# Kernel optimization log

Hardware: AMD Instinct MI355X
Metric: run time of the kernel (lower is better)

Reference implementation:

```python
import jax, jax.numpy as jnp
import numpy as np

# Skeleton structure (start, end) connections
REAL_CONNECTIONS = [(0,1),(1,2),(2,3),(3,4),(1,5),(5,6),(6,7),(7,8),(8,9),(8,13),(8,17),(8,21),(8,25),(9,10),(10,11),(11,12),(13,14),(14,15),(15,16),(17,18),(18,19),(19,20),(21,22),(22,23),(23,24),(25,26),(26,27),(27,28),(4,29),(29,30),(29,34),(29,38),(29,42),(29,46),(30,31),(31,32),(32,33),(34,35),(35,36),(36,37),(38,39),(39,40),(40,41),(42,43),(43,44),(44,45),(46,47),(47,48),(48,49)]

def _bone_ranges():
    # dict insertion order matters only for iteration; result is a sum so order-free
    ranges = {(0,1):(0.05,0.15),(1,2):(0.1,0.2),(1,5):(0.1,0.2),(2,3):(0.2,0.35),(3,4):(0.2,0.35),(5,6):(0.2,0.35),(6,7):(0.2,0.35),(4,8):(0.05,0.15),(7,29):(0.05,0.15)}
    for s, e in REAL_CONNECTIONS:
        if 8 <= s < 50 and 8 <= e < 50:
            ranges[(s, e)] = (0.01, 0.08)
    return ranges

_BR = _bone_ranges()
BONE_S = np.array([k[0] for k in _BR], np.int32)
BONE_E = np.array([k[1] for k in _BR], np.int32)
BONE_MIN = np.array([v[0] for v in _BR.values()], np.float32)
BONE_MAX = np.array([v[1] for v in _BR.values()], np.float32)

SYM_L = np.array([8 + i for i in range(21)] + [2, 3, 4], np.int32)
SYM_R = np.array([29 + i for i in range(21)] + [5, 6, 7], np.int32)

ANG_A = np.array([1, 1, 2, 5], np.int32)
ANG_B = np.array([2, 5, 3, 6], np.int32)
ANG_C = np.array([3, 6, 4, 7], np.int32)

CONN_S = np.array([c[0] for c in REAL_CONNECTIONS], np.int32)
CONN_E = np.array([c[1] for c in REAL_CONNECTIONS], np.int32)

DEG = np.float32(180.0 / np.pi)
EPS = np.float32(1e-12)

def _relu(x):
    return jnp.maximum(x, 0.0)

def _normalize(v):
    n = jnp.linalg.norm(v, axis=-1, keepdims=True)
    return v / jnp.maximum(n, EPS)

def setup_inputs() -> dict:
    key = jax.random.key(0)
    k1, k2 = jax.random.split(key)
    B, S, D = 64, 2048, 150
    pred_poses = jax.random.normal(k1, (B, S, D), dtype=jnp.float32)
    target_poses = jax.random.normal(k2, (B, S, D), dtype=jnp.float32)
    return {"pred_poses": pred_poses, "target_poses": target_poses}

def reference(pred_poses, target_poses):
    B, S, _ = pred_poses.shape
    J = pred_poses.reshape(B, S, 50, 3)
    T = target_poses.reshape(B, S, 50, 3)

    # ---- bone length loss (49 constrained bones, one gathered pass) ----
    bv = J[:, :, BONE_E] - J[:, :, BONE_S]                 # [B,S,49,3]
    bl = jnp.linalg.norm(bv, axis=-1)                      # [B,S,49]
    bone_pen = _relu(bl - BONE_MAX) + _relu(BONE_MIN - bl)
    bone_loss = bone_pen.mean()  # == sum over bones of per-bone mean / n_bones

    # ---- joint angle loss (4 triples) ----
    v1 = _normalize(J[:, :, ANG_A] - J[:, :, ANG_B])       # [B,S,4,3]
    v2 = _normalize(J[:, :, ANG_C] - J[:, :, ANG_B])
    cos = jnp.clip(jnp.sum(v1 * v2, axis=-1), -1.0, 1.0)
    deg = jnp.arccos(cos) * DEG
    angle_loss = (_relu(30.0 - deg) + _relu(deg - 150.0)).mean()

    # ---- symmetry loss (24 pairs) ----
    L = J[:, :, SYM_L]                                     # [B,S,24,3]
    R = J[:, :, SYM_R]
    x_sym = jnp.abs(L[..., 0] + R[..., 0])                 # [B,S,24]
    yz_sim = jnp.abs(L[..., 1:] - R[..., 1:]).mean(axis=-1)
    symmetry_loss = (x_sym + yz_sim).mean()

    # ---- temporal consistency ----
    vel = J[:, 1:] - J[:, :-1]                             # [B,S-1,50,3]
    acc = vel[:, 1:] - vel[:, :-1]
    temporal_loss = jnp.linalg.norm(acc, axis=-1).mean() + 0.5 * jnp.linalg.norm(vel, axis=-1).mean()

    # ---- supervised bone-length consistency (all 49 connections) ----
    tb = jnp.linalg.norm(T[:, :, CONN_E] - T[:, :, CONN_S], axis=-1)
    pb = jnp.linalg.norm(J[:, :, CONN_E] - J[:, :, CONN_S], axis=-1)
    supervised_loss = jnp.abs(pb - tb).mean()

    total = (1.0 * bone_loss + 0.5 * angle_loss + 0.3 * symmetry_loss
             + 0.2 * temporal_loss + supervised_loss)
    return bone_loss, angle_loss, symmetry_loss, temporal_loss, supervised_loss, total
```

## Files before the change

### kernel.cpp

```cpp
#include <hip/hip_runtime.h>
#include <math.h>

#define TPB 512
#define CH  32
#define CPB 8

static constexpr int B_     = 64;
static constexpr int S_     = 2048;
static constexpr int TOTAL  = B_ * S_;
static constexpr int NCHUNK = TOTAL / CH;
static constexpr int NBLK   = NCHUNK / CPB;
static constexpr int SAMPB  = 600;
static constexpr int PREDB  = (CH + 2) * SAMPB;
static constexpr int TGTB   = CH * SAMPB;
static constexpr int CHB    = PREDB + TGTB;
static constexpr int NSLICE = 39;
static constexpr int BUFB   = NSLICE * 1024;
static constexpr long TOTB  = (long)TOTAL * SAMPB;

__constant__ int US_[51] = {0,1,1,2,3,5,6,4,7,7,4,
    8,8,8,8,8,9,10,11,13,14,
    15,17,18,19,21,22,23,25,26,27,
    29,29,29,29,29,30,31,32,34,35,
    36,38,39,40,42,43,44,46,47,48};
__constant__ int UE_[51] = {1,2,5,3,4,6,7,8,29,8,29,
    9,13,17,21,25,10,11,12,14,15,
    16,18,19,20,22,23,24,26,27,28,
    30,34,38,42,46,31,32,33,35,36,
    37,39,40,41,43,44,45,47,48,49};
__constant__ float UMIN11_[11] = {0.05f,0.1f,0.1f,0.2f,0.2f,0.2f,0.2f,0.05f,0.05f,-1e9f,-1e9f};
__constant__ float UMAX11_[11] = {0.15f,0.2f,0.2f,0.35f,0.35f,0.35f,0.35f,0.15f,0.15f,1e9f,1e9f};
__constant__ float WSUP11_[11] = {1.f,1.f,1.f,1.f,1.f,1.f,1.f,0.f,0.f,1.f,1.f};
__constant__ int SL_[24] = {8,9,10,11,12,13,14,15,16,17,18,19,20,21,22,23,24,25,26,27,28,2,3,4};
__constant__ int SR_[24] = {29,30,31,32,33,34,35,36,37,38,39,40,41,42,43,44,45,46,47,48,49,5,6,7};
__constant__ int AJ_[4] = {1,1,2,5};
__constant__ int BJ_[4] = {2,5,3,6};
__constant__ int CJ_[4] = {3,6,4,7};

struct F3 { float x, y, z; };
__device__ __forceinline__ F3 ld3(const float* p) { return *(const F3*)p; }
#define SQRTF __builtin_amdgcn_sqrtf

typedef const __attribute__((address_space(1))) void* gas_t;
typedef __attribute__((address_space(3))) void* las_t;

__global__ __launch_bounds__(TPB, 4) void pose_main(
    const float* __restrict__ pred, const float* __restrict__ tgt,
    float* __restrict__ part)
{
    __shared__ __align__(16) char LDS[2 * BUFB];

    const int tid = threadIdx.x;
    const int blk = blockIdx.x;
    const int li  = tid & 15;
    const int g   = tid >> 4;

    const int   uOs0 = US_[g] * 3, uOe0 = UE_[g] * 3;
    const float uMn0 = (g < 11) ? UMIN11_[g] : 0.01f;
    const float uMx0 = (g < 11) ? UMAX11_[g] : 0.08f;
    const float uW0  = (g < 11) ? WSUP11_[g] : 1.f;
    const bool  u1_on = (g < 19);
    const int   k1   = u1_on ? g + 32 : 50;
    const int   uOs1 = US_[k1] * 3, uOe1 = UE_[k1] * 3;
    const bool sy_on = (g < 24);
    const int  ksy = sy_on ? g : 0;
    const int  syL = SL_[ksy] * 3, syR = SR_[ksy] * 3;
    const int aAo = AJ_[g & 3] * 3, aBo = BJ_[g & 3] * 3, aCo = CJ_[g & 3] * 3;
    const int  tO0 = g * 3;
    const int  tO1 = (g + 32) * 3;
    const bool t1_on = (g < 18);

    float a_bone = 0.f, a_ang = 0.f, a_sym = 0.f, a_vel = 0.f, a_acc = 0.f, a_sup = 0.f;

    const int w      = tid >> 6;
    const int lane16 = (tid & 63) << 4;
    auto stage = [&](int cidx, char* lbuf) {
        const long nb = (long)cidx * TGTB;
        const char* pb = (const char*)pred + nb;
        const char* tb = (const char*)tgt  + nb - PREDB;
        const long prem = TOTB - nb - 16;
        #pragma unroll
        for (int s = 0; s < 5; ++s) {
            const int slice = w + s * 8;
            if (slice < NSLICE) {
                const long o = (long)slice * 1024 + lane16;
                const char* src = (o < PREDB)
                    ? pb + (o > prem ? prem : o)
                    : tb + (o > (long)(CHB - 16) ? (long)(CHB - 16) : o);
                __builtin_amdgcn_global_load_lds((gas_t)src, (las_t)(lbuf + slice * 1024), 16, 0, 0);
            }
        }
    };

    const int c0 = blk * CPB;
    stage(c0, LDS);

    #pragma unroll
    for (int c = 0; c < CPB; ++c) {
        char* curb = LDS + (c & 1) * BUFB;
        char* nxtb = LDS + ((c & 1) ^ 1) * BUFB;
        if (c + 1 < CPB) {
            stage(c0 + c + 1, nxtb);
            if (w < 7) asm volatile("s_waitcnt vmcnt(5)" ::: "memory");
            else       asm volatile("s_waitcnt vmcnt(4)" ::: "memory");
        } else {
            asm volatile("s_waitcnt vmcnt(0)" ::: "memory");
        }
        __builtin_amdgcn_s_barrier();
        __builtin_amdgcn_sched_barrier(0);

        const float* Jl = (const float*)curb;
        const float* Tl = Jl + PREDB / 4;
        const int s_base = ((c0 + c) * CH) & (S_ - 1);

        #pragma unroll
        for (int h = 0; h < 2; ++h) {
            const int sb = (li + h * 16) * 150;
            const float* Jp = Jl + sb;
            const float* Tp = Tl + sb;

            auto edge = [&](int so, int eo, float mn, float mx, float wsup) {
                const F3 je = ld3(Jp + eo), js = ld3(Jp + so);
                const float dx = je.x - js.x, dy = je.y - js.y, dz = je.z - js.z;
                const float pb = SQRTF(dx * dx + dy * dy + dz * dz);
                a_bone += fmaxf(pb - mx, 0.f) + fmaxf(mn - pb, 0.f);
                const F3 te = ld3(Tp + eo), ts = ld3(Tp + so);
                const float tx = te.x - ts.x, ty = te.y - ts.y, tz = te.z - ts.z;
                const float tb = SQRTF(tx * tx + ty * ty + tz * tz);
                a_sup += wsup * fabsf(pb - tb);
            };
            edge(uOs0, uOe0, uMn0, uMx0, uW0);
            if (u1_on) edge(uOs1, uOe1, 0.01f, 0.08f, 1.f);

            if (sy_on) {
                const F3 L = ld3(Jp + syL), R = ld3(Jp + syR);
                a_sym += fabsf(L.x + R.x) + 0.5f * (fabsf(L.y - R.y) + fabsf(L.z - R.z));
            }

            if (g < 4) {
                const F3 A = ld3(Jp + aAo), Bb = ld3(Jp + aBo), C = ld3(Jp + aCo);
                const float v1x = A.x - Bb.x, v1y = A.y - Bb.y, v1z = A.z - Bb.z;
                const float v2x = C.x - Bb.x, v2y = C.y - Bb.y, v2z = C.z - Bb.z;
                const float n12 = (v1x*v1x + v1y*v1y + v1z*v1z) * (v2x*v2x + v2y*v2y + v2z*v2z);
                const float inv = __frsqrt_rn(fmaxf(n12, 1e-24f));
                float cosv = (v1x*v2x + v1y*v2y + v1z*v2z) * inv;
                cosv = fminf(fmaxf(cosv, -1.f), 1.f);
                const float deg = acosf(cosv) * 57.29577951308232f;
                a_ang += fmaxf(30.f - deg, 0.f) + fmaxf(deg - 150.f, 0.f);
            }

            {
                const int sidx = s_base + li + h * 16;
                const bool v_ok = sidx < S_ - 1;
                const bool a_ok = sidx < S_ - 2;
                auto temporal = [&](int off) {
                    const F3 p0 = ld3(Jp + off), p1 = ld3(Jp + off + 150), p2 = ld3(Jp + off + 300);
                    if (v_ok) {
                        const float vx = p1.x - p0.x, vy = p1.y - p0.y, vz = p1.z - p0.z;
                        a_vel += SQRTF(vx*vx + vy*vy + vz*vz);
                        if (a_ok) {
                            const float ax = p2.x - 2.f*p1.x + p0.x;
                            const float ay = p2.y - 2.f*p1.y + p0.y;
                            const float az = p2.z - 2.f*p1.z + p0.z;
                            a_acc += SQRTF(ax*ax + ay*ay + az*az);
                        }
                    }
                };
                temporal(tO0);
                if (t1_on) temporal(tO1);
            }
        }

        asm volatile("" ::: "memory");
        __builtin_amdgcn_s_barrier();
    }

    float vals[6] = {a_bone, a_ang, a_sym, a_vel, a_acc, a_sup};
    #pragma unroll
    for (int k = 0; k < 6; ++k)
        #pragma unroll
        for (int off = 32; off > 0; off >>= 1)
            vals[k] += __shfl_down(vals[k], off, 64);

    float* red = (float*)LDS;
    const int lane = tid & 63;
    if (lane == 0) {
        #pragma unroll
        for (int k = 0; k < 6; ++k) red[w * 6 + k] = vals[k];
    }
    __syncthreads();
    if (tid == 0) {
        #pragma unroll
        for (int k = 0; k < 6; ++k) {
            float s = 0.f;
            #pragma unroll
            for (int v = 0; v < 8; ++v) s += red[v * 6 + k];
            part[k * NBLK + blk] = s;
        }
    }
}

__global__ __launch_bounds__(256) void pose_reduce(
    const float* __restrict__ part, float* __restrict__ out)
{
    __shared__ float red[4][6];
    const int tid = threadIdx.x;
    float a[6];
    #pragma unroll
    for (int k = 0; k < 6; ++k) {
        float s = 0.f;
        for (int i = tid; i < NBLK; i += 256) s += part[k * NBLK + i];
        a[k] = s;
    }
    #pragma unroll
    for (int k = 0; k < 6; ++k)
        #pragma unroll
        for (int off = 32; off > 0; off >>= 1)
            a[k] += __shfl_down(a[k], off, 64);

    const int wid = tid >> 6, lane = tid & 63;
    if (lane == 0) {
        #pragma unroll
        for (int k = 0; k < 6; ++k) red[wid][k] = a[k];
    }
    __syncthreads();
    if (tid == 0) {
        float t[6];
        #pragma unroll
        for (int k = 0; k < 6; ++k) t[k] = red[0][k] + red[1][k] + red[2][k] + red[3][k];
        const float bone = t[0] * (1.f / ((float)TOTAL * 49.f));
        const float ang  = t[1] * (1.f / ((float)TOTAL * 4.f));
        const float sym  = t[2] * (1.f / ((float)TOTAL * 24.f));
        const float temporal = t[4] * (1.f / ((float)B_ * (float)(S_ - 2) * 50.f))
                             + 0.5f * t[3] * (1.f / ((float)B_ * (float)(S_ - 1) * 50.f));
        const float sup  = t[5] * (1.f / ((float)TOTAL * 49.f));
        out[0] = bone;
        out[1] = ang;
        out[2] = sym;
        out[3] = temporal;
        out[4] = sup;
        out[5] = bone + 0.5f * ang + 0.3f * sym + 0.2f * temporal + sup;
    }
}

extern "C" void kernel_launch(void* const* d_in, const int* in_sizes, int n_in,
                              void* d_out, int out_size, void* d_ws, size_t ws_size,
                              hipStream_t stream)
{
    const float* pred = (const float*)d_in[0];
    const float* tgt  = (const float*)d_in[1];
    float* part = (float*)d_ws;
    pose_main<<<NBLK, TPB, 0, stream>>>(pred, tgt, part);
    pose_reduce<<<1, 256, 0, stream>>>(part, (float*)d_out);
}
```

Before: 39.64 us.

## Double block and chunk size and give each thread group one edge task

Blocks grow to 1024 threads and each chunk to 64 samples, with 77 LDS slices per double-buffer half. Work is remapped so each 16-lane group handles at most one edge and one temporal joint. The four angle terms move to otherwise idle groups 60–63. The aim is to remove the second edge and temporal pass per thread and cut the two-sample halo overhead per chunk. In exchange it uses about 157 KB of LDS per block, which limits residency to one block per CU, and keeps a launch bound of 4 blocks that cannot be met at this size.

```diff
diff --git a/kernel.cpp b/kernel.cpp
--- a/kernel.cpp
+++ b/kernel.cpp
@@ -1,8 +1,8 @@
 #include <hip/hip_runtime.h>
 #include <math.h>
 
-#define TPB 512
-#define CH  32
+#define TPB 1024
+#define CH  64
 #define CPB 8
 
 static constexpr int B_     = 64;
@@ -14,7 +14,7 @@
 static constexpr int PREDB  = (CH + 2) * SAMPB;
 static constexpr int TGTB   = CH * SAMPB;
 static constexpr int CHB    = PREDB + TGTB;
-static constexpr int NSLICE = 39;
+static constexpr int NSLICE = 77;
 static constexpr int BUFB   = NSLICE * 1024;
 static constexpr long TOTB  = (long)TOTAL * SAMPB;
 
@@ -55,20 +55,20 @@
     const int li  = tid & 15;
     const int g   = tid >> 4;
 
-    const int   uOs0 = US_[g] * 3, uOe0 = UE_[g] * 3;
-    const float uMn0 = (g < 11) ? UMIN11_[g] : 0.01f;
-    const float uMx0 = (g < 11) ? UMAX11_[g] : 0.08f;
-    const float uW0  = (g < 11) ? WSUP11_[g] : 1.f;
-    const bool  u1_on = (g < 19);
-    const int   k1   = u1_on ? g + 32 : 50;
-    const int   uOs1 = US_[k1] * 3, uOe1 = UE_[k1] * 3;
+    const bool u_on = (g < 51);
+    const int  gu   = u_on ? g : 0;
+    const int  uOs = US_[gu] * 3, uOe = UE_[gu] * 3;
+    const float uMn = (gu < 11) ? UMIN11_[gu] : 0.01f;
+    const float uMx = (gu < 11) ? UMAX11_[gu] : 0.08f;
+    const float uW  = (gu < 11) ? WSUP11_[gu] : 1.f;
     const bool sy_on = (g < 24);
     const int  ksy = sy_on ? g : 0;
     const int  syL = SL_[ksy] * 3, syR = SR_[ksy] * 3;
-    const int aAo = AJ_[g & 3] * 3, aBo = BJ_[g & 3] * 3, aCo = CJ_[g & 3] * 3;
+    const bool an_on = (g >= 60);
+    const int  ka  = (g - 60) & 3;
+    const int  aAo = AJ_[ka] * 3, aBo = BJ_[ka] * 3, aCo = CJ_[ka] * 3;
+    const bool t_on = (g < 50);
     const int  tO0 = g * 3;
-    const int  tO1 = (g + 32) * 3;
-    const bool t1_on = (g < 18);
 
     float a_bone = 0.f, a_ang = 0.f, a_sym = 0.f, a_vel = 0.f, a_acc = 0.f, a_sup = 0.f;
 
@@ -81,7 +81,7 @@
         const long prem = TOTB - nb - 16;
         #pragma unroll
         for (int s = 0; s < 5; ++s) {
-            const int slice = w + s * 8;
+            const int slice = w + s * 16;
             if (slice < NSLICE) {
                 const long o = (long)slice * 1024 + lane16;
                 const char* src = (o < PREDB)
@@ -101,8 +101,8 @@
         char* nxtb = LDS + ((c & 1) ^ 1) * BUFB;
         if (c + 1 < CPB) {
             stage(c0 + c + 1, nxtb);
-            if (w < 7) asm volatile("s_waitcnt vmcnt(5)" ::: "memory");
-            else       asm volatile("s_waitcnt vmcnt(4)" ::: "memory");
+            if (w < 13) asm volatile("s_waitcnt vmcnt(5)" ::: "memory");
+            else        asm volatile("s_waitcnt vmcnt(4)" ::: "memory");
         } else {
             asm volatile("s_waitcnt vmcnt(0)" ::: "memory");
         }
@@ -114,30 +114,28 @@
         const int s_base = ((c0 + c) * CH) & (S_ - 1);
 
         #pragma unroll
-        for (int h = 0; h < 2; ++h) {
+        for (int h = 0; h < 4; ++h) {
             const int sb = (li + h * 16) * 150;
             const float* Jp = Jl + sb;
             const float* Tp = Tl + sb;
 
-            auto edge = [&](int so, int eo, float mn, float mx, float wsup) {
-                const F3 je = ld3(Jp + eo), js = ld3(Jp + so);
+            if (u_on) {
+                const F3 je = ld3(Jp + uOe), js = ld3(Jp + uOs);
                 const float dx = je.x - js.x, dy = je.y - js.y, dz = je.z - js.z;
                 const float pb = SQRTF(dx * dx + dy * dy + dz * dz);
-                a_bone += fmaxf(pb - mx, 0.f) + fmaxf(mn - pb, 0.f);
-                const F3 te = ld3(Tp + eo), ts = ld3(Tp + so);
+                a_bone += fmaxf(pb - uMx, 0.f) + fmaxf(uMn - pb, 0.f);
+                const F3 te = ld3(Tp + uOe), ts = ld3(Tp + uOs);
                 const float tx = te.x - ts.x, ty = te.y - ts.y, tz = te.z - ts.z;
                 const float tb = SQRTF(tx * tx + ty * ty + tz * tz);
-                a_sup += wsup * fabsf(pb - tb);
-            };
-            edge(uOs0, uOe0, uMn0, uMx0, uW0);
-            if (u1_on) edge(uOs1, uOe1, 0.01f, 0.08f, 1.f);
+                a_sup += uW * fabsf(pb - tb);
+            }
 
             if (sy_on) {
                 const F3 L = ld3(Jp + syL), R = ld3(Jp + syR);
                 a_sym += fabsf(L.x + R.x) + 0.5f * (fabsf(L.y - R.y) + fabsf(L.z - R.z));
             }
 
-            if (g < 4) {
+            if (an_on) {
                 const F3 A = ld3(Jp + aAo), Bb = ld3(Jp + aBo), C = ld3(Jp + aCo);
                 const float v1x = A.x - Bb.x, v1y = A.y - Bb.y, v1z = A.z - Bb.z;
                 const float v2x = C.x - Bb.x, v2y = C.y - Bb.y, v2z = C.z - Bb.z;
@@ -149,25 +147,21 @@
                 a_ang += fmaxf(30.f - deg, 0.f) + fmaxf(deg - 150.f, 0.f);
             }
 
-            {
+            if (t_on) {
                 const int sidx = s_base + li + h * 16;
                 const bool v_ok = sidx < S_ - 1;
                 const bool a_ok = sidx < S_ - 2;
-                auto temporal = [&](int off) {
-                    const F3 p0 = ld3(Jp + off), p1 = ld3(Jp + off + 150), p2 = ld3(Jp + off + 300);
-                    if (v_ok) {
-                        const float vx = p1.x - p0.x, vy = p1.y - p0.y, vz = p1.z - p0.z;
-                        a_vel += SQRTF(vx*vx + vy*vy + vz*vz);
-                        if (a_ok) {
-                            const float ax = p2.x - 2.f*p1.x + p0.x;
-                            const float ay = p2.y - 2.f*p1.y + p0.y;
-                            const float az = p2.z - 2.f*p1.z + p0.z;
-                            a_acc += SQRTF(ax*ax + ay*ay + az*az);
-                        }
+                const F3 p0 = ld3(Jp + tO0), p1 = ld3(Jp + tO0 + 150), p2 = ld3(Jp + tO0 + 300);
+                if (v_ok) {
+                    const float vx = p1.x - p0.x, vy = p1.y - p0.y, vz = p1.z - p0.z;
+                    a_vel += SQRTF(vx*vx + vy*vy + vz*vz);
+                    if (a_ok) {
+                        const float ax = p2.x - 2.f*p1.x + p0.x;
+                        const float ay = p2.y - 2.f*p1.y + p0.y;
+                        const float az = p2.z - 2.f*p1.z + p0.z;
+                        a_acc += SQRTF(ax*ax + ay*ay + az*az);
                     }
-                };
-                temporal(tO0);
-                if (t1_on) temporal(tO1);
+                }
             }
         }
 
@@ -194,7 +188,7 @@
         for (int k = 0; k < 6; ++k) {
             float s = 0.f;
             #pragma unroll
-            for (int v = 0; v < 8; ++v) s += red[v * 6 + k];
+            for (int v = 0; v < 16; ++v) s += red[v * 6 + k];
             part[k * NBLK + blk] = s;
         }
     }
```

Result: faster. 37.99 us, median of 2 (-4.2%).
